# Performance work log

Hardware: AMD Instinct MI355X
Metric: run time of the kernel (lower is better)

## Reference

```python
import jax, jax.numpy as jnp
import numpy as np

B, C, H, W = 8, 256, 64, 64
G = min(C // 4, 32)  # 32 groups, as in the torch module
EPS = 1e-6


def setup_inputs() -> dict:
    key = jax.random.key(0)
    ks = jax.random.split(key, 12)
    s = 1.0 / np.sqrt(C)
    inp = {
        "x": jax.random.normal(ks[0], (B, C, H, W), jnp.float32),
        "gn_scale": 1.0 + 0.02 * jax.random.normal(ks[1], (C,), jnp.float32),
        "gn_bias": 0.02 * jax.random.normal(ks[2], (C,), jnp.float32),
        "w_q": s * jax.random.normal(ks[3], (C, C), jnp.float32),
        "b_q": 0.01 * jax.random.normal(ks[4], (C,), jnp.float32),
        "w_k": s * jax.random.normal(ks[5], (C, C), jnp.float32),
        "b_k": 0.01 * jax.random.normal(ks[6], (C,), jnp.float32),
        "w_v": s * jax.random.normal(ks[7], (C, C), jnp.float32),
        "b_v": 0.01 * jax.random.normal(ks[8], (C,), jnp.float32),
        "w_o": s * jax.random.normal(ks[9], (C, C), jnp.float32),
        "b_o": 0.01 * jax.random.normal(ks[10], (C,), jnp.float32),
    }
    return inp


def _group_norm(x, scale, bias):
    b, c, h, w = x.shape
    xg = x.reshape(b, G, c // G, h, w)
    m = jnp.mean(xg, axis=(2, 3, 4), keepdims=True)
    v = jnp.var(xg, axis=(2, 3, 4), keepdims=True)
    xn = ((xg - m) * jax.lax.rsqrt(v + EPS)).reshape(b, c, h, w)
    return xn * scale[None, :, None, None] + bias[None, :, None, None]


def _nin(h, w, b):
    # 1x1 conv: [B,C,H,W] x [out,in] -> [B,out,H,W]
    return jnp.einsum('bchw,oc->bohw', h, w) + b[None, :, None, None]


def reference(x, gn_scale, gn_bias, w_q, b_q, w_k, b_k, w_v, b_v, w_o, b_o):
    b, c, h, w = x.shape
    n = h * w
    hn = _group_norm(x, gn_scale, gn_bias)
    q = _nin(hn, w_q, b_q).reshape(b, c, n)
    k = _nin(hn, w_k, b_k).reshape(b, c, n)
    v = _nin(hn, w_v, b_v).reshape(b, c, n)
    scale = jnp.asarray(c, x.dtype) ** -0.5
    att = jax.nn.softmax(jnp.einsum('bcn,bcm->bnm', q, k) * scale, axis=-1)
    out = jnp.einsum('bnm,bcm->bcn', att, v).reshape(b, c, h, w)
    out = _nin(out, w_o, b_o)
    return (x + out) / jnp.asarray(np.sqrt(2.0), x.dtype)
```

## Files before the change

### kernel.cpp

```cpp
#include <hip/hip_runtime.h>

typedef __attribute__((ext_vector_type(8))) short bf16x8;
typedef __attribute__((ext_vector_type(4))) float f32x4;
typedef unsigned short us;
typedef unsigned char u8;
typedef long i64;

#define MFMA(a, b, c) __builtin_amdgcn_mfma_f32_16x16x32_bf16((a), (b), (c), 0, 0, 0)
#define MFMA8(a, b, c) __builtin_amdgcn_mfma_f32_16x16x32_fp8_fp8((a), (b), (c), 0, 0, 0)

__device__ __forceinline__ us f2bf(float f) {
  union { float f; unsigned int u; } x; x.f = f;
  return (us)((x.u + 0x7FFFu + ((x.u >> 16) & 1u)) >> 16);
}
__device__ __forceinline__ u8 f2fp8(float f) {
  return (u8)(__builtin_amdgcn_cvt_pk_fp8_f32(f, f, 0, false) & 0xFF);
}

__device__ __forceinline__ void glds16(const us* g, us* l) {
  __builtin_amdgcn_global_load_lds(
      (const __attribute__((address_space(1))) unsigned int*)g,
      (__attribute__((address_space(3))) unsigned int*)l, 16, 0, 0);
}

__global__ __launch_bounds__(256) void conv_w(const float* __restrict__ a, const float* __restrict__ b,
                                              const float* __restrict__ c, const float* __restrict__ d,
                                              us* __restrict__ oa, us* __restrict__ ob,
                                              us* __restrict__ oc, us* __restrict__ od) {
  int i = blockIdx.x * 256 + threadIdx.x;
  oa[i] = f2bf(a[i]); ob[i] = f2bf(b[i]); oc[i] = f2bf(c[i]); od[i] = f2bf(d[i]);
}

__global__ __launch_bounds__(256) void gn_kernel(const float* __restrict__ x,
                                                 const float* __restrict__ scale,
                                                 const float* __restrict__ bias,
                                                 us* __restrict__ hnT) {
  int b = blockIdx.y, g = blockIdx.x;
  int tid = threadIdx.x;
  int c0 = g * 8;
  const float* xb = x + (((size_t)b * 256 + c0) << 12);
  float s = 0.f, sq = 0.f;
  for (int j = 0; j < 8; ++j) {
    const float* xc = xb + ((size_t)j << 12);
    for (int n = tid; n < 4096; n += 256) {
      float v = xc[n];
      s += v; sq += v * v;
    }
  }
  for (int off = 32; off; off >>= 1) { s += __shfl_xor(s, off); sq += __shfl_xor(sq, off); }
  __shared__ float red[8];
  int w = tid >> 6, lane = tid & 63;
  if (lane == 0) { red[w] = s; red[4 + w] = sq; }
  __syncthreads();
  s  = red[0] + red[1] + red[2] + red[3];
  sq = red[4] + red[5] + red[6] + red[7];
  float mean = s * (1.f / 32768.f);
  float var  = sq * (1.f / 32768.f) - mean * mean;
  float rstd = rsqrtf(var + 1e-6f);
  float aa[8], bb[8];
  for (int j = 0; j < 8; ++j) {
    float sc = scale[c0 + j] * rstd;
    aa[j] = sc; bb[j] = bias[c0 + j] - mean * sc;
  }
  us* dst = hnT + ((size_t)b << 12) * 256 + c0;
  for (int n = tid; n < 4096; n += 256) {
    union { us u16[8]; uint4 v; } t;
    for (int j = 0; j < 8; ++j) {
      float v = xb[((size_t)j << 12) + n];
      t.u16[j] = f2bf(v * aa[j] + bb[j]);
    }
    *(uint4*)(dst + (size_t)n * 256) = t.v;
  }
}

__global__ __launch_bounds__(256) void proj_nk(const us* __restrict__ hnT,
                                               const us* __restrict__ wq, const us* __restrict__ wk,
                                               const float* __restrict__ bq, const float* __restrict__ bk,
                                               u8* __restrict__ q8, u8* __restrict__ k8) {
  __shared__ __align__(16) us smem[2 * 128 * 64];
  us* A_s = smem;
  us* B_s = smem + 128 * 64;
  int bx = blockIdx.x, by = blockIdx.y;
  int tid = threadIdx.x, w = tid >> 6, lane = tid & 63;
  int l15 = lane & 15, quad = lane >> 4;
  const us* wsrc; const float* bsrc; u8* dst; int o0;
  if (by < 2) { wsrc = wq; bsrc = bq; dst = q8; o0 = by * 128; }
  else        { wsrc = wk; bsrc = bk; dst = k8; o0 = (by - 2) * 128; }
  size_t R0 = (size_t)bx * 128;
  int wm = (w & 1) * 64, wn = (w >> 1) * 64;
  f32x4 z = {0.f, 0.f, 0.f, 0.f};
  f32x4 acc[4][4] = {{z,z,z,z},{z,z,z,z},{z,z,z,z},{z,z,z,z}};

  for (int kk = 0; kk < 256; kk += 64) {
    __syncthreads();
#pragma unroll
    for (int j = 0; j < 4; ++j) {
      int cidx = j * 256 + tid;
      int row = cidx >> 3, cc = cidx & 7;
      int gch = (cc ^ (row & 7)) * 8;
      glds16(hnT + (R0 + row) * 256 + kk + gch, A_s + cidx * 8);
      glds16(wsrc + (size_t)(o0 + row) * 256 + kk + gch, B_s + cidx * 8);
    }
    __syncthreads();
#pragma unroll
    for (int k2 = 0; k2 < 2; ++k2) {
      int ch = (k2 * 4 + quad) ^ (l15 & 7);
      bf16x8 af[4], bf[4];
#pragma unroll
      for (int i = 0; i < 4; ++i) {
        af[i] = *(const bf16x8*)(A_s + (wm + i * 16 + l15) * 64 + ch * 8);
        bf[i] = *(const bf16x8*)(B_s + (wn + i * 16 + l15) * 64 + ch * 8);
      }
#pragma unroll
      for (int i = 0; i < 4; ++i)
#pragma unroll
        for (int j = 0; j < 4; ++j)
          acc[i][j] = MFMA(af[i], bf[j], acc[i][j]);
    }
  }
  __syncthreads();
  u8* T = (u8*)smem;
#pragma unroll
  for (int j = 0; j < 4; ++j) {
    float bv = bsrc[o0 + wn + j * 16 + l15];
#pragma unroll
    for (int i = 0; i < 4; ++i)
#pragma unroll
      for (int r = 0; r < 4; ++r)
        T[(wm + i * 16 + quad * 4 + r) * 144 + wn + j * 16 + l15] = f2fp8(acc[i][j][r] + bv);
  }
  __syncthreads();
  int row = tid >> 1, half = tid & 1;
  const u8* src = T + row * 144 + half * 64;
  u8* gd = dst + (R0 + row) * 256 + o0 + half * 64;
#pragma unroll
  for (int k = 0; k < 4; ++k)
    *(uint4*)(gd + k * 16) = *(const uint4*)(src + k * 16);
}

__global__ __launch_bounds__(256) void proj_cn(const us* __restrict__ A,
                                               const us* __restrict__ Bm,
                                               const float* __restrict__ bias,
                                               const float* __restrict__ x,
                                               float* __restrict__ outf,
                                               u8* __restrict__ out8, int mode) {
  __shared__ __align__(16) us smem[2 * 128 * 64];
  us* A_s = smem;
  us* B_s = smem + 128 * 64;
  int bx = blockIdx.x, bb = blockIdx.y;
  int mt = bx & 1, ntile = bx >> 1;
  int tid = threadIdx.x, w = tid >> 6, lane = tid & 63;
  int l15 = lane & 15, quad = lane >> 4;
  int R0 = mt * 128;
  size_t NB = (size_t)bb * 4096 + ntile * 128;
  int wm = (w & 1) * 64, wn = (w >> 1) * 64;
  f32x4 z = {0.f, 0.f, 0.f, 0.f};
  f32x4 acc[4][4] = {{z,z,z,z},{z,z,z,z},{z,z,z,z},{z,z,z,z}};

  for (int kk = 0; kk < 256; kk += 64) {
    __syncthreads();
#pragma unroll
    for (int j = 0; j < 4; ++j) {
      int cidx = j * 256 + tid;
      int row = cidx >> 3, cc = cidx & 7;
      int gch = (cc ^ (row & 7)) * 8;
      glds16(A + (size_t)(R0 + row) * 256 + kk + gch, A_s + cidx * 8);
      glds16(Bm + (NB + row) * 256 + kk + gch, B_s + cidx * 8);
    }
    __syncthreads();
#pragma unroll
    for (int k2 = 0; k2 < 2; ++k2) {
      int ch = (k2 * 4 + quad) ^ (l15 & 7);
      bf16x8 af[4], bf[4];
#pragma unroll
      for (int i = 0; i < 4; ++i) {
        af[i] = *(const bf16x8*)(A_s + (wm + i * 16 + l15) * 64 + ch * 8);
        bf[i] = *(const bf16x8*)(B_s + (wn + i * 16 + l15) * 64 + ch * 8);
      }
#pragma unroll
      for (int i = 0; i < 4; ++i)
#pragma unroll
        for (int j = 0; j < 4; ++j)
          acc[i][j] = MFMA(af[i], bf[j], acc[i][j]);
    }
  }
  const float is2 = 0.70710678118654752f;
  if (mode == 0) {
    __syncthreads();
    u8* T = (u8*)smem;
#pragma unroll
    for (int i = 0; i < 4; ++i)
#pragma unroll
      for (int r = 0; r < 4; ++r) {
        int cl = wm + i * 16 + quad * 4 + r;
        float bv = bias[R0 + cl];
#pragma unroll
        for (int j = 0; j < 4; ++j)
          T[cl * 144 + wn + j * 16 + l15] = f2fp8(acc[i][j][r] + bv);
      }
    __syncthreads();
    int row = tid >> 1, half = tid & 1;
    const u8* src = T + row * 144 + half * 64;
    u8* gd = out8 + (((size_t)bb * 256 + R0 + row) << 12) + ntile * 128 + half * 64;
#pragma unroll
    for (int k = 0; k < 4; ++k)
      *(uint4*)(gd + k * 16) = *(const uint4*)(src + k * 16);
  } else {
#pragma unroll
    for (int i = 0; i < 4; ++i)
#pragma unroll
      for (int r = 0; r < 4; ++r) {
        int c = R0 + wm + i * 16 + quad * 4 + r;
        float bv = bias[c];
        size_t base = (((size_t)bb * 256 + c) << 12) + (ntile * 128 + wn);
#pragma unroll
        for (int j = 0; j < 4; ++j) {
          size_t idx = base + j * 16 + l15;
          outf[idx] = (x[idx] + acc[i][j][r] + bv) * is2;
        }
      }
  }
}

__global__ __launch_bounds__(256) void attn_partial(const u8* __restrict__ q8,
                                                    const u8* __restrict__ k8,
                                                    const u8* __restrict__ v8,
                                                    float* __restrict__ Of,
                                                    us* __restrict__ Ob,
                                                    float* __restrict__ l0,
                                                    float* __restrict__ l1) {
  int b = blockIdx.y, nt = blockIdx.x, h = blockIdx.z;
  int tid = threadIdx.x, w = tid >> 6, lane = tid & 63;
  int l15 = lane & 15, quad = lane >> 4;
  __shared__ u8 kt_s[32 * 256];
  __shared__ u8 v_s[256 * 48];
  __shared__ u8 p_s[4 * 16 * 40];
  const u8* qb = q8 + ((size_t)b << 12) * 256;
  const u8* kb = k8 + ((size_t)b << 12) * 256;
  const u8* vb = v8 + ((size_t)b << 12) * 256;
  int n0 = nt * 64 + w * 16;
  int m_base = h * 2048;
  i64 qf[8];
#pragma unroll
  for (int ks = 0; ks < 8; ++ks)
    qf[ks] = *(const i64*)(qb + (size_t)(n0 + l15) * 256 + ks * 32 + quad * 8);
  f32x4 z = {0.f, 0.f, 0.f, 0.f};
  f32x4 of[16];
#pragma unroll
  for (int i = 0; i < 16; ++i) of[i] = z;
  float lrow[4] = {0.f, 0.f, 0.f, 0.f};

  int km = tid >> 4, kj = tid & 15;
  int km2 = km + 16;
  int ksw = (kj ^ (km & 15)) * 16;
  int vc = tid;

  uint4 kr0 = *(const uint4*)(kb + (size_t)(m_base + km) * 256 + kj * 16);
  uint4 kr1 = *(const uint4*)(kb + (size_t)(m_base + km2) * 256 + kj * 16);
  uint4 vr0 = *(const uint4*)(vb + ((size_t)vc << 12) + m_base);
  uint4 vr1 = *(const uint4*)(vb + ((size_t)vc << 12) + m_base + 16);

  for (int mt = 0; mt < 64; ++mt) {
    __syncthreads();
    *(uint4*)(kt_s + km * 256 + ksw) = kr0;
    *(uint4*)(kt_s + km2 * 256 + ksw) = kr1;
    *(uint4*)(v_s + vc * 48) = vr0;
    *(uint4*)(v_s + vc * 48 + 16) = vr1;
    __syncthreads();
    if (mt < 63) {
      int mn = m_base + (mt + 1) * 32;
      kr0 = *(const uint4*)(kb + (size_t)(mn + km) * 256 + kj * 16);
      kr1 = *(const uint4*)(kb + (size_t)(mn + km2) * 256 + kj * 16);
      vr0 = *(const uint4*)(vb + ((size_t)vc << 12) + mn);
      vr1 = *(const uint4*)(vb + ((size_t)vc << 12) + mn + 16);
    }

    f32x4 s0 = z, s1 = z;
    int r0 = l15, r1 = 16 + l15;
#pragma unroll
    for (int ks = 0; ks < 8; ++ks) {
      int ch = ks * 2 + (quad >> 1), half = (quad & 1) * 8;
      i64 k0 = *(const i64*)(kt_s + r0 * 256 + ((ch ^ (r0 & 15)) * 16) + half);
      i64 k1 = *(const i64*)(kt_s + r1 * 256 + ((ch ^ (r1 & 15)) * 16) + half);
      s0 = MFMA8(qf[ks], k0, s0);
      s1 = MFMA8(qf[ks], k1, s1);
    }

    const float sc = 0.0625f;
    u8* pw = p_s + w * 640;
#pragma unroll
    for (int r = 0; r < 4; ++r) {
      float p0 = __expf(fminf(s0[r] * sc, 5.9f));
      float p1 = __expf(fminf(s1[r] * sc, 5.9f));
      lrow[r] += p0 + p1;
      int pk = __builtin_amdgcn_cvt_pk_fp8_f32(p0, p1, 0, false);
      int n = quad * 4 + r;
      pw[n * 40 + l15]      = (u8)(pk & 0xFF);
      pw[n * 40 + 16 + l15] = (u8)((pk >> 8) & 0xFF);
    }
    i64 pf = *(const i64*)(pw + l15 * 40 + quad * 8);

#pragma unroll
    for (int cs = 0; cs < 16; ++cs) {
      i64 vf = *(const i64*)(v_s + (cs * 16 + l15) * 48 + quad * 8);
      of[cs] = MFMA8(pf, vf, of[cs]);
    }
  }

  size_t obase = ((size_t)b << 12) * 256;
#pragma unroll
  for (int r = 0; r < 4; ++r) {
    int n = n0 + quad * 4 + r;
    float l = lrow[r];
    l += __shfl_xor(l, 1);
    l += __shfl_xor(l, 2);
    l += __shfl_xor(l, 4);
    l += __shfl_xor(l, 8);
    size_t row = obase + (size_t)n * 256;
    if (h == 0) {
      if (l15 == 0) l0[((size_t)b << 12) + n] = l;
#pragma unroll
      for (int cs = 0; cs < 16; ++cs)
        Of[row + cs * 16 + l15] = of[cs][r];
    } else {
      if (l15 == 0) l1[((size_t)b << 12) + n] = l;
#pragma unroll
      for (int cs = 0; cs < 16; ++cs)
        Ob[row + cs * 16 + l15] = f2bf(of[cs][r]);
    }
  }
}

__global__ __launch_bounds__(256) void combine(const float* __restrict__ Of,
                                               const us* __restrict__ Ob,
                                               const float* __restrict__ l0,
                                               const float* __restrict__ l1,
                                               us* __restrict__ attT) {
  int idx = blockIdx.x * 256 + threadIdx.x;
  int row = idx >> 5;
  int c0 = (idx & 31) * 8;
  size_t base = (size_t)row * 256 + c0;
  float inv = 1.f / (l0[row] + l1[row]);
  float4 f0 = *(const float4*)(Of + base);
  float4 f1 = *(const float4*)(Of + base + 4);
  union { us u16[8]; uint4 v; } pb;
  pb.v = *(const uint4*)(Ob + base);
  union { us u16[8]; uint4 v; } t;
  float fo[8] = {f0.x, f0.y, f0.z, f0.w, f1.x, f1.y, f1.z, f1.w};
#pragma unroll
  for (int j = 0; j < 8; ++j) {
    union { unsigned int u; float f; } bu; bu.u = ((unsigned int)pb.u16[j]) << 16;
    t.u16[j] = f2bf((fo[j] + bu.f) * inv);
  }
  *(uint4*)(attT + base) = t.v;
}

extern "C" void kernel_launch(void* const* d_in, const int* in_sizes, int n_in,
                              void* d_out, int out_size, void* d_ws, size_t ws_size,
                              hipStream_t stream) {
  const float* x  = (const float*)d_in[0];
  const float* gs = (const float*)d_in[1];
  const float* gb = (const float*)d_in[2];
  const float* wq = (const float*)d_in[3];
  const float* bq = (const float*)d_in[4];
  const float* wk = (const float*)d_in[5];
  const float* bk = (const float*)d_in[6];
  const float* wv = (const float*)d_in[7];
  const float* bv = (const float*)d_in[8];
  const float* wo = (const float*)d_in[9];
  const float* bo = (const float*)d_in[10];
  float* out = (float*)d_out;

  us* ws = (us*)d_ws;
  const size_t SZ = (size_t)8 * 4096 * 256;
  us* hnT = ws;
  u8* q8  = (u8*)(ws + SZ);
  u8* k8  = q8 + SZ;
  u8* v8  = k8 + SZ;
  us* wqb = (us*)(v8 + SZ);
  us* wkb = wqb + 65536;
  us* wvb = wkb + 65536;
  us* wob = wvb + 65536;
  float* l0 = (float*)(wob + 65536);
  float* l1 = l0 + 32768;
  float* Opart0 = out;
  us* Opart1 = hnT;
  us* attT = (us*)q8;

  conv_w<<<256, 256, 0, stream>>>(wq, wk, wv, wo, wqb, wkb, wvb, wob);
  gn_kernel<<<dim3(32, 8), 256, 0, stream>>>(x, gs, gb, hnT);
  proj_nk<<<dim3(256, 4), 256, 0, stream>>>(hnT, wqb, wkb, bq, bk, q8, k8);
  proj_cn<<<dim3(64, 8), 256, 0, stream>>>(wvb, hnT, bv, nullptr, nullptr, v8, 0);
  attn_partial<<<dim3(64, 8, 2), 256, 0, stream>>>(q8, k8, v8, Opart0, Opart1, l0, l1);
  combine<<<4096, 256, 0, stream>>>(Opart0, Opart1, l0, l1, attT);
  proj_cn<<<dim3(64, 8), 256, 0, stream>>>(wob, attT, bo, x, out, nullptr, 1);
}
```

Measured before the change: 427.9 us.

## Fuse split-attention combine into output projection and store both partials as bf16

Removes the separate combine kernel. The output projection now loads both bf16 attention partials, sums them, scales by the inverse softmax denominator, and writes the result into shared memory in place of the async global-to-LDS load. Both partial outputs are now stored as bf16 rather than one in fp32, which halves that write traffic but adds rounding. The group-norm kernel also moves to 512 threads per block. The fused path gives up the asynchronous LDS load for synchronous register loads in the final GEMM.

After: 369.1 us. 13.7% less time.

```diff
diff --git a/kernel.cpp b/kernel.cpp
--- a/kernel.cpp
+++ b/kernel.cpp
@@ -12,6 +12,10 @@
 __device__ __forceinline__ us f2bf(float f) {
   union { float f; unsigned int u; } x; x.f = f;
   return (us)((x.u + 0x7FFFu + ((x.u >> 16) & 1u)) >> 16);
+}
+__device__ __forceinline__ float bf2f(us v) {
+  union { unsigned int u; float f; } x; x.u = ((unsigned int)v) << 16;
+  return x.f;
 }
 __device__ __forceinline__ u8 f2fp8(float f) {
   return (u8)(__builtin_amdgcn_cvt_pk_fp8_f32(f, f, 0, false) & 0xFF);
@@ -31,7 +35,7 @@
   oa[i] = f2bf(a[i]); ob[i] = f2bf(b[i]); oc[i] = f2bf(c[i]); od[i] = f2bf(d[i]);
 }
 
-__global__ __launch_bounds__(256) void gn_kernel(const float* __restrict__ x,
+__global__ __launch_bounds__(512) void gn_kernel(const float* __restrict__ x,
                                                  const float* __restrict__ scale,
                                                  const float* __restrict__ bias,
                                                  us* __restrict__ hnT) {
@@ -42,18 +46,18 @@
   float s = 0.f, sq = 0.f;
   for (int j = 0; j < 8; ++j) {
     const float* xc = xb + ((size_t)j << 12);
-    for (int n = tid; n < 4096; n += 256) {
+    for (int n = tid; n < 4096; n += 512) {
       float v = xc[n];
       s += v; sq += v * v;
     }
   }
   for (int off = 32; off; off >>= 1) { s += __shfl_xor(s, off); sq += __shfl_xor(sq, off); }
-  __shared__ float red[8];
+  __shared__ float red[16];
   int w = tid >> 6, lane = tid & 63;
-  if (lane == 0) { red[w] = s; red[4 + w] = sq; }
+  if (lane == 0) { red[w] = s; red[8 + w] = sq; }
   __syncthreads();
-  s  = red[0] + red[1] + red[2] + red[3];
-  sq = red[4] + red[5] + red[6] + red[7];
+  s = 0.f; sq = 0.f;
+  for (int j = 0; j < 8; ++j) { s += red[j]; sq += red[8 + j]; }
   float mean = s * (1.f / 32768.f);
   float var  = sq * (1.f / 32768.f) - mean * mean;
   float rstd = rsqrtf(var + 1e-6f);
@@ -63,7 +67,7 @@
     aa[j] = sc; bb[j] = bias[c0 + j] - mean * sc;
   }
   us* dst = hnT + ((size_t)b << 12) * 256 + c0;
-  for (int n = tid; n < 4096; n += 256) {
+  for (int n = tid; n < 4096; n += 512) {
     union { us u16[8]; uint4 v; } t;
     for (int j = 0; j < 8; ++j) {
       float v = xb[((size_t)j << 12) + n];
@@ -143,7 +147,11 @@
                                                const float* __restrict__ bias,
                                                const float* __restrict__ x,
                                                float* __restrict__ outf,
-                                               u8* __restrict__ out8, int mode) {
+                                               u8* __restrict__ out8,
+                                               const us* __restrict__ Ob1,
+                                               const float* __restrict__ l0,
+                                               const float* __restrict__ l1,
+                                               int mode) {
   __shared__ __align__(16) us smem[2 * 128 * 64];
   us* A_s = smem;
   us* B_s = smem + 128 * 64;
@@ -157,6 +165,15 @@
   f32x4 z = {0.f, 0.f, 0.f, 0.f};
   f32x4 acc[4][4] = {{z,z,z,z},{z,z,z,z},{z,z,z,z},{z,z,z,z}};
 
+  float inv_[4];
+  if (mode == 1) {
+#pragma unroll
+    for (int j = 0; j < 4; ++j) {
+      int row = (j * 256 + tid) >> 3;
+      inv_[j] = 1.f / (l0[NB + row] + l1[NB + row]);
+    }
+  }
+
   for (int kk = 0; kk < 256; kk += 64) {
     __syncthreads();
 #pragma unroll
@@ -165,7 +182,19 @@
       int row = cidx >> 3, cc = cidx & 7;
       int gch = (cc ^ (row & 7)) * 8;
       glds16(A + (size_t)(R0 + row) * 256 + kk + gch, A_s + cidx * 8);
-      glds16(Bm + (NB + row) * 256 + kk + gch, B_s + cidx * 8);
+      if (mode == 0) {
+        glds16(Bm + (NB + row) * 256 + kk + gch, B_s + cidx * 8);
+      } else {
+        size_t gi = (NB + row) * 256 + kk + gch;
+        union { us q[8]; uint4 v; } o0, o1, t;
+        o0.v = *(const uint4*)(Bm + gi);
+        o1.v = *(const uint4*)(Ob1 + gi);
+        float inv = inv_[j];
+#pragma unroll
+        for (int e = 0; e < 8; ++e)
+          t.q[e] = f2bf((bf2f(o0.q[e]) + bf2f(o1.q[e])) * inv);
+        *(uint4*)(B_s + cidx * 8) = t.v;
+      }
     }
     __syncthreads();
 #pragma unroll
@@ -225,8 +254,8 @@
 __global__ __launch_bounds__(256) void attn_partial(const u8* __restrict__ q8,
                                                     const u8* __restrict__ k8,
                                                     const u8* __restrict__ v8,
-                                                    float* __restrict__ Of,
-                                                    us* __restrict__ Ob,
+                                                    us* __restrict__ Ob0,
+                                                    us* __restrict__ Ob1,
                                                     float* __restrict__ l0,
                                                     float* __restrict__ l1) {
   int b = blockIdx.y, nt = blockIdx.x, h = blockIdx.z;
@@ -307,6 +336,8 @@
     }
   }
 
+  us* dst = (h == 0) ? Ob0 : Ob1;
+  float* ldst = (h == 0) ? l0 : l1;
   size_t obase = ((size_t)b << 12) * 256;
 #pragma unroll
   for (int r = 0; r < 4; ++r) {
@@ -316,43 +347,12 @@
     l += __shfl_xor(l, 2);
     l += __shfl_xor(l, 4);
     l += __shfl_xor(l, 8);
+    if (l15 == 0) ldst[((size_t)b << 12) + n] = l;
     size_t row = obase + (size_t)n * 256;
-    if (h == 0) {
-      if (l15 == 0) l0[((size_t)b << 12) + n] = l;
-#pragma unroll
-      for (int cs = 0; cs < 16; ++cs)
-        Of[row + cs * 16 + l15] = of[cs][r];
-    } else {
-      if (l15 == 0) l1[((size_t)b << 12) + n] = l;
-#pragma unroll
-      for (int cs = 0; cs < 16; ++cs)
-        Ob[row + cs * 16 + l15] = f2bf(of[cs][r]);
-    }
-  }
-}
-
-__global__ __launch_bounds__(256) void combine(const float* __restrict__ Of,
-                                               const us* __restrict__ Ob,
-                                               const float* __restrict__ l0,
-                                               const float* __restrict__ l1,
-                                               us* __restrict__ attT) {
-  int idx = blockIdx.x * 256 + threadIdx.x;
-  int row = idx >> 5;
-  int c0 = (idx & 31) * 8;
-  size_t base = (size_t)row * 256 + c0;
-  float inv = 1.f / (l0[row] + l1[row]);
-  float4 f0 = *(const float4*)(Of + base);
-  float4 f1 = *(const float4*)(Of + base + 4);
-  union { us u16[8]; uint4 v; } pb;
-  pb.v = *(const uint4*)(Ob + base);
-  union { us u16[8]; uint4 v; } t;
-  float fo[8] = {f0.x, f0.y, f0.z, f0.w, f1.x, f1.y, f1.z, f1.w};
-#pragma unroll
-  for (int j = 0; j < 8; ++j) {
-    union { unsigned int u; float f; } bu; bu.u = ((unsigned int)pb.u16[j]) << 16;
-    t.u16[j] = f2bf((fo[j] + bu.f) * inv);
-  }
-  *(uint4*)(attT + base) = t.v;
+#pragma unroll
+    for (int cs = 0; cs < 16; ++cs)
+      dst[row + cs * 16 + l15] = f2bf(of[cs][r]);
+  }
 }
 
 extern "C" void kernel_launch(void* const* d_in, const int* in_sizes, int n_in,
@@ -383,15 +383,15 @@
   us* wob = wvb + 65536;
   float* l0 = (float*)(wob + 65536);
   float* l1 = l0 + 32768;
-  float* Opart0 = out;
-  us* Opart1 = hnT;
-  us* attT = (us*)q8;
+  us* Ob0 = (us*)(l1 + 32768);
+  us* Ob1 = hnT;
 
   conv_w<<<256, 256, 0, stream>>>(wq, wk, wv, wo, wqb, wkb, wvb, wob);
-  gn_kernel<<<dim3(32, 8), 256, 0, stream>>>(x, gs, gb, hnT);
+  gn_kernel<<<dim3(32, 8), 512, 0, stream>>>(x, gs, gb, hnT);
   proj_nk<<<dim3(256, 4), 256, 0, stream>>>(hnT, wqb, wkb, bq, bk, q8, k8);
-  proj_cn<<<dim3(64, 8), 256, 0, stream>>>(wvb, hnT, bv, nullptr, nullptr, v8, 0);
-  attn_partial<<<dim3(64, 8, 2), 256, 0, stream>>>(q8, k8, v8, Opart0, Opart1, l0, l1);
-  combine<<<4096, 256, 0, stream>>>(Opart0, Opart1, l0, l1, attT);
-  proj_cn<<<dim3(64, 8), 256, 0, stream>>>(wob, attT, bo, x, out, nullptr, 1);
-}
+  proj_cn<<<dim3(64, 8), 256, 0, stream>>>(wvb, hnT, bv, nullptr, nullptr, v8,
+                                           nullptr, nullptr, nullptr, 0);
+  attn_partial<<<dim3(64, 8, 2), 256, 0, stream>>>(q8, k8, v8, Ob0, Ob1, l0, l1);
+  proj_cn<<<dim3(64, 8), 256, 0, stream>>>(wob, Ob0, bo, x, out, nullptr,
+                                           Ob1, l0, l1, 1);
+}
```
